# Performance work log

Hardware: AMD Instinct MI355X
Metric: run time of the kernel (lower is better)

Reference implementation:

```python
import jax, jax.numpy as jnp
import numpy as np

N_NODES = 20000
N_EDGES = 160000
D_IN = 512
D_OUT = 64


def _propagate(x, src, dst, num_nodes):
    # SLPropagate with add_self_loops=False, normalize=False:
    # out[dst] += x[src]  (plain sum aggregation over incoming edges)
    return jax.ops.segment_sum(x[src], dst, num_segments=num_nodes)


def setup_inputs() -> dict:
    key = jax.random.key(0)
    k1, k2, k3, k4 = jax.random.split(key, 4)
    x = jax.random.normal(k1, (N_NODES, D_IN), dtype=jnp.float32)
    edge_index = jax.random.randint(k2, (2, N_EDGES), 0, N_NODES, dtype=jnp.int64)
    # torch.nn.Linear default init scale ~ 1/sqrt(fan_in)
    s = 1.0 / np.sqrt(D_IN)
    W1 = jax.random.uniform(k3, (D_IN, D_IN), dtype=jnp.float32, minval=-s, maxval=s)
    W2 = jax.random.uniform(k4, (D_OUT, D_IN), dtype=jnp.float32, minval=-s, maxval=s)
    return {"x": x, "edge_index": edge_index, "W1": W1, "W2": W2}


def reference(x, edge_index, W1, W2):
    num_nodes = x.shape[0]
    src, dst = edge_index[0], edge_index[1]
    h = _propagate(x, src, dst, num_nodes)          # [N, D_IN]
    h = jax.nn.relu(jnp.einsum('nd,ed->ne', h, W1))  # lin1 (no bias) + relu
    h = _propagate(h, src, dst, num_nodes)          # [N, D_IN]
    h = jnp.einsum('nd,od->no', h, W2)              # lin2 (no bias) -> [N, D_OUT]
    return jax.nn.log_softmax(h, axis=1)
```

## Files before the change

kernel.cpp:

```cpp
#include <hip/hip_runtime.h>

#define D 512
#define DOUT 64

typedef __bf16 bf16x8 __attribute__((ext_vector_type(8)));
typedef float floatx4 __attribute__((ext_vector_type(4)));

__device__ __forceinline__ void async_cp16(const void* g, void* lds) {
    __builtin_amdgcn_global_load_lds(
        (__attribute__((address_space(1))) void*)(void*)g,
        (__attribute__((address_space(3))) void*)lds, 16, 0, 0);
}

__global__ __launch_bounds__(256) void misc_kernel(
        const int* __restrict__ dst, int* __restrict__ deg, int nE, int degBlocks,
        const float* __restrict__ x, __bf16* __restrict__ xb, int xN8,
        const float* __restrict__ W1, __bf16* __restrict__ w1b, int w1N8,
        const float* __restrict__ W2, __bf16* __restrict__ w2b, int w2N8) {
    int b = blockIdx.x;
    if (b < degBlocks) {
        int e = b * 256 + threadIdx.x;
        if (e < nE) atomicAdd(&deg[dst[e]], 1);
        return;
    }
    b -= degBlocks;
    int xBlocks = (xN8 + 255) >> 8;
    int w1Blocks = (w1N8 + 255) >> 8;
    const float* in; __bf16* outp; int n8;
    if (b < xBlocks) { in = x; outp = xb; n8 = xN8; }
    else if (b < xBlocks + w1Blocks) { b -= xBlocks; in = W1; outp = w1b; n8 = w1N8; }
    else { b -= xBlocks + w1Blocks; in = W2; outp = w2b; n8 = w2N8; }
    int i = b * 256 + threadIdx.x;
    if (i < n8) {
        const float4* p = (const float4*)in + (size_t)i * 2;
        float4 v0 = p[0], v1 = p[1];
        bf16x8 o;
        o[0] = (__bf16)v0.x; o[1] = (__bf16)v0.y; o[2] = (__bf16)v0.z; o[3] = (__bf16)v0.w;
        o[4] = (__bf16)v1.x; o[5] = (__bf16)v1.y; o[6] = (__bf16)v1.z; o[7] = (__bf16)v1.w;
        *((bf16x8*)outp + i) = o;
    }
}

__global__ __launch_bounds__(1024) void exscan_kernel(const int* __restrict__ deg,
                                                      int* __restrict__ rp,
                                                      int* __restrict__ cursor, int n) {
    __shared__ int wtot[16];
    __shared__ int carry;
    int tid = threadIdx.x, lane = tid & 63, wid = tid >> 6;
    if (tid == 0) carry = 0;
    __syncthreads();
    for (int base = 0; base < n; base += 4096) {
        int i4 = base + tid * 4;
        int4 v = make_int4(0, 0, 0, 0);
        if (i4 + 3 < n) v = *(const int4*)(deg + i4);
        else {
            if (i4 + 0 < n) v.x = deg[i4 + 0];
            if (i4 + 1 < n) v.y = deg[i4 + 1];
            if (i4 + 2 < n) v.z = deg[i4 + 2];
            if (i4 + 3 < n) v.w = deg[i4 + 3];
        }
        int tsum = v.x + v.y + v.z + v.w;
        int s = tsum;
        #pragma unroll
        for (int off = 1; off < 64; off <<= 1) {
            int t = __shfl_up(s, off, 64);
            if (lane >= off) s += t;
        }
        if (lane == 63) wtot[wid] = s;
        __syncthreads();
        if (wid == 0 && lane < 16) {
            int wv = wtot[lane];
            int ws_ = wv;
            #pragma unroll
            for (int off = 1; off < 16; off <<= 1) {
                int t = __shfl_up(ws_, off, 64);
                if (lane >= off) ws_ += t;
            }
            wtot[lane] = ws_ - wv;
        }
        __syncthreads();
        int excl = carry + wtot[wid] + (s - tsum);
        int4 o;
        o.x = excl; o.y = o.x + v.x; o.z = o.y + v.y; o.w = o.z + v.z;
        if (i4 + 3 < n) {
            *(int4*)(rp + i4) = o;
            *(int4*)(cursor + i4) = o;
        } else {
            if (i4 + 0 < n) { rp[i4 + 0] = o.x; cursor[i4 + 0] = o.x; }
            if (i4 + 1 < n) { rp[i4 + 1] = o.y; cursor[i4 + 1] = o.y; }
            if (i4 + 2 < n) { rp[i4 + 2] = o.z; cursor[i4 + 2] = o.z; }
            if (i4 + 3 < n) { rp[i4 + 3] = o.w; cursor[i4 + 3] = o.w; }
        }
        __syncthreads();
        if (tid == 1023) carry = o.w + v.w;
        __syncthreads();
    }
    if (tid == 0) rp[n] = carry;
}

__global__ void fill_kernel(const int* __restrict__ src, const int* __restrict__ dst,
                            int* __restrict__ cursor, int* __restrict__ col, int nE) {
    int e = blockIdx.x * blockDim.x + threadIdx.x;
    if (e < nE) {
        int d = dst[e];
        int p = atomicAdd(&cursor[d], 1);
        col[p] = src[e];
    }
}

template<int BM, int BN, int WR, int WC, bool RELU>
__global__ __launch_bounds__(256) void gemm_mfma_nt(
        const __bf16* __restrict__ A, const __bf16* __restrict__ B,
        __bf16* __restrict__ Cout, int M, int N, int K) {
    constexpr int BK = 32;
    constexpr int WM = BM / WR, WN = BN / WC;
    constexpr int MI = WM / 16, NI = WN / 16;
    constexpr int CPA = BM / 64, CPB = BN / 64;

    __shared__ __bf16 As[4 * BM * 8];
    __shared__ __bf16 Bs[4 * BN * 8];

    const int tid = threadIdx.x;
    const int w = tid >> 6, lane = tid & 63;
    const int wrow = w / WC, wcol = w % WC;
    const int m0 = blockIdx.y * BM, n0 = blockIdx.x * BN;
    const int quad = lane >> 4, l15 = lane & 15;

    floatx4 acc[MI][NI] = {};

    for (int k0 = 0; k0 < K; k0 += BK) {
        #pragma unroll
        for (int c = 0; c < CPA; ++c) {
            int ca = w * CPA + c;
            int kq = ca / CPA;
            int row = m0 + (ca % CPA) * 64 + lane;
            if (row > M - 1) row = M - 1;
            async_cp16(A + (size_t)row * K + k0 + kq * 8, &As[(size_t)ca * 512]);
        }
        #pragma unroll
        for (int c = 0; c < CPB; ++c) {
            int cb = w * CPB + c;
            int kq = cb / CPB;
            int nn = n0 + (cb % CPB) * 64 + lane;
            async_cp16(B + (size_t)nn * K + k0 + kq * 8, &Bs[(size_t)cb * 512]);
        }
        __syncthreads();

        bf16x8 af[MI], bfr[NI];
        #pragma unroll
        for (int mi = 0; mi < MI; ++mi)
            af[mi] = *(const bf16x8*)&As[(size_t)(quad * BM + wrow * WM + mi * 16 + l15) * 8];
        #pragma unroll
        for (int nj = 0; nj < NI; ++nj)
            bfr[nj] = *(const bf16x8*)&Bs[(size_t)(quad * BN + wcol * WN + nj * 16 + l15) * 8];
        #pragma unroll
        for (int mi = 0; mi < MI; ++mi)
            #pragma unroll
            for (int nj = 0; nj < NI; ++nj)
                acc[mi][nj] = __builtin_amdgcn_mfma_f32_16x16x32_bf16(
                    af[mi], bfr[nj], acc[mi][nj], 0, 0, 0);
        __syncthreads();
    }

    #pragma unroll
    for (int mi = 0; mi < MI; ++mi) {
        #pragma unroll
        for (int r = 0; r < 4; ++r) {
            int m = m0 + wrow * WM + mi * 16 + quad * 4 + r;
            if (m < M) {
                #pragma unroll
                for (int nj = 0; nj < NI; ++nj) {
                    int n = n0 + wcol * WN + nj * 16 + l15;
                    float v = acc[mi][nj][r];
                    if (RELU) v = fmaxf(v, 0.f);
                    Cout[(size_t)m * N + n] = (__bf16)v;
                }
            }
        }
    }
}

__global__ __launch_bounds__(256) void prop1_gemm2(
        const __bf16* __restrict__ t, const int* __restrict__ rp,
        const int* __restrict__ col, const __bf16* __restrict__ B,
        __bf16* __restrict__ u, int nN) {
    __shared__ __bf16 As[32 * 512];
    __shared__ __bf16 Bs[4 * 64 * 8];

    const int tid = threadIdx.x;
    const int w = tid >> 6, lane = tid & 63;
    const int quad = lane >> 4, l15 = lane & 15;
    const int wrow = w >> 1, wcol = w & 1;
    const int m0 = blockIdx.x * 32;

    for (int r = w; r < 32; r += 4) {
        int n = m0 + r;
        float acc0[8] = {}, acc1[8] = {};
        if (n < nN) {
            int s0 = rp[n], s1 = rp[n + 1];
            int e = s0;
            for (; e + 4 <= s1; e += 4) {
                int sa = col[e], sb = col[e + 1], sc = col[e + 2], sd = col[e + 3];
                bf16x8 va = *(const bf16x8*)(t + (size_t)sa * D + lane * 8);
                bf16x8 vb = *(const bf16x8*)(t + (size_t)sb * D + lane * 8);
                bf16x8 vc = *(const bf16x8*)(t + (size_t)sc * D + lane * 8);
                bf16x8 vd = *(const bf16x8*)(t + (size_t)sd * D + lane * 8);
                #pragma unroll
                for (int i = 0; i < 8; ++i) {
                    acc0[i] += (float)va[i] + (float)vc[i];
                    acc1[i] += (float)vb[i] + (float)vd[i];
                }
            }
            for (; e < s1; ++e) {
                int sa = col[e];
                bf16x8 va = *(const bf16x8*)(t + (size_t)sa * D + lane * 8);
                #pragma unroll
                for (int i = 0; i < 8; ++i) acc0[i] += (float)va[i];
            }
        }
        bf16x8 o;
        #pragma unroll
        for (int i = 0; i < 8; ++i) o[i] = (__bf16)fmaxf(acc0[i] + acc1[i], 0.f);
        int P = r * 64 + ((lane + r) & 63);
        *(bf16x8*)&As[(size_t)P * 8] = o;
    }
    __syncthreads();

    floatx4 acc[2] = {};
    for (int k0 = 0; k0 < D; k0 += 32) {
        async_cp16(B + (size_t)lane * D + k0 + w * 8, &Bs[(size_t)w * 512]);
        __syncthreads();
        int g = (k0 >> 3) + quad;
        int row = wrow * 16 + l15;
        bf16x8 af = *(const bf16x8*)&As[(size_t)(row * 64 + ((g + row) & 63)) * 8];
        #pragma unroll
        for (int nj = 0; nj < 2; ++nj) {
            bf16x8 bfr = *(const bf16x8*)&Bs[(size_t)(quad * 64 + wcol * 32 + nj * 16 + l15) * 8];
            acc[nj] = __builtin_amdgcn_mfma_f32_16x16x32_bf16(af, bfr, acc[nj], 0, 0, 0);
        }
        __syncthreads();
    }

    #pragma unroll
    for (int r = 0; r < 4; ++r) {
        int m = m0 + wrow * 16 + quad * 4 + r;
        if (m < nN) {
            #pragma unroll
            for (int nj = 0; nj < 2; ++nj)
                u[(size_t)m * DOUT + wcol * 32 + nj * 16 + l15] = (__bf16)acc[nj][r];
        }
    }
}

__global__ __launch_bounds__(256) void prop2_lsm(const __bf16* __restrict__ u,
        const int* __restrict__ rp, const int* __restrict__ col,
        float* __restrict__ out, int nN) {
    int n = blockIdx.x * 4 + (threadIdx.x >> 6);
    if (n >= nN) return;
    int lane = threadIdx.x & 63;
    int s0 = rp[n], s1 = rp[n + 1];
    float a0 = 0.f, a1 = 0.f, a2 = 0.f, a3 = 0.f;
    int e = s0;
    for (; e + 4 <= s1; e += 4) {
        int sa = col[e], sb = col[e + 1], sc = col[e + 2], sd = col[e + 3];
        a0 += (float)u[(size_t)sa * DOUT + lane];
        a1 += (float)u[(size_t)sb * DOUT + lane];
        a2 += (float)u[(size_t)sc * DOUT + lane];
        a3 += (float)u[(size_t)sd * DOUT + lane];
    }
    for (; e < s1; ++e) a0 += (float)u[(size_t)col[e] * DOUT + lane];
    float v = (a0 + a2) + (a1 + a3);
    float mx = v;
    #pragma unroll
    for (int off = 32; off >= 1; off >>= 1) mx = fmaxf(mx, __shfl_xor(mx, off, 64));
    float s = expf(v - mx);
    #pragma unroll
    for (int off = 32; off >= 1; off >>= 1) s += __shfl_xor(s, off, 64);
    out[(size_t)n * DOUT + lane] = v - mx - logf(s);
}


extern "C" void kernel_launch(void* const* d_in, const int* in_sizes, int n_in,
                              void* d_out, int out_size, void* d_ws, size_t ws_size,
                              hipStream_t stream) {
    const float* x  = (const float*)d_in[0];
    const int*   ei = (const int*)d_in[1];
    const float* W1 = (const float*)d_in[2];
    const float* W2 = (const float*)d_in[3];
    float* out = (float*)d_out;

    const int N = in_sizes[0] / D;
    const int E = in_sizes[1] / 2;
    const int* src = ei;
    const int* dst = ei + E;

    size_t off = 0;
    auto alloc = [&](size_t bytes) -> void* {
        void* p = (char*)d_ws + off;
        off = (off + bytes + 255) & ~(size_t)255;
        return p;
    };
    int*    deg     = (int*)alloc(sizeof(int) * (size_t)N);
    int*    row_ptr = (int*)alloc(sizeof(int) * (size_t)(N + 1));
    int*    cursor  = (int*)alloc(sizeof(int) * (size_t)N);
    int*    col     = (int*)alloc(sizeof(int) * (size_t)E);
    __bf16* w1b     = (__bf16*)alloc(sizeof(__bf16) * (size_t)D * D);
    __bf16* w2b     = (__bf16*)alloc(sizeof(__bf16) * (size_t)DOUT * D);
    __bf16* xb      = (__bf16*)alloc(sizeof(__bf16) * (size_t)N * D);
    __bf16* t       = (__bf16*)alloc(sizeof(__bf16) * (size_t)N * D);
    __bf16* u       = (__bf16*)alloc(sizeof(__bf16) * (size_t)N * DOUT);

    const int degBlocks = (E + 255) / 256;
    const int xN8 = N * D / 8, w1N8 = D * D / 8, w2N8 = DOUT * D / 8;
    const int cvtBlocks = (xN8 + 255) / 256 + (w1N8 + 255) / 256 + (w2N8 + 255) / 256;

    hipMemsetAsync(deg, 0, sizeof(int) * (size_t)N, stream);
    misc_kernel<<<degBlocks + cvtBlocks, 256, 0, stream>>>(
        dst, deg, E, degBlocks, x, xb, xN8, W1, w1b, w1N8, W2, w2b, w2N8);
    exscan_kernel<<<1, 1024, 0, stream>>>(deg, row_ptr, cursor, N);
    fill_kernel<<<(E + 255) / 256, 256, 0, stream>>>(src, dst, cursor, col, E);

    dim3 g1(D / 128, (N + 127) / 128);
    gemm_mfma_nt<128, 128, 2, 2, false><<<g1, 256, 0, stream>>>(xb, w1b, t, N, D, D);
    prop1_gemm2<<<(N + 31) / 32, 256, 0, stream>>>(t, row_ptr, col, w2b, u, N);
    prop2_lsm<<<(N + 3) / 4, 256, 0, stream>>>(u, row_ptr, col, out, N);
}
```

Measured before the change: 186.0 us.

## Fold degree histogram into GEMM1 launch and halve prop1 tile rows

Replaces the memset with in-kernel zeroing of the degree array inside the conversion kernel. The edge-degree histogram moves out of the conversion kernel into extra blocks of the first GEMM launch, so the atomics overlap with MFMA work. The GEMM is also flattened to a 1D grid. The fused propagate+GEMM2 kernel now handles 16 nodes per block instead of 32, giving twice as many blocks and less LDS per block, at the cost of reloading W2 tiles more often.

```diff
diff --git a/kernel.cpp b/kernel.cpp
--- a/kernel.cpp
+++ b/kernel.cpp
@@ -12,18 +12,23 @@
         (__attribute__((address_space(3))) void*)lds, 16, 0, 0);
 }
 
-__global__ __launch_bounds__(256) void misc_kernel(
-        const int* __restrict__ dst, int* __restrict__ deg, int nE, int degBlocks,
+__global__ __launch_bounds__(256) void prep_kernel(
+        int* __restrict__ deg, int nN, int zeroBlocks,
         const float* __restrict__ x, __bf16* __restrict__ xb, int xN8,
         const float* __restrict__ W1, __bf16* __restrict__ w1b, int w1N8,
         const float* __restrict__ W2, __bf16* __restrict__ w2b, int w2N8) {
     int b = blockIdx.x;
-    if (b < degBlocks) {
-        int e = b * 256 + threadIdx.x;
-        if (e < nE) atomicAdd(&deg[dst[e]], 1);
+    if (b < zeroBlocks) {
+        int i4 = b * 1024 + threadIdx.x * 4;
+        if (i4 + 3 < nN) *(int4*)(deg + i4) = make_int4(0, 0, 0, 0);
+        else {
+            if (i4 + 0 < nN) deg[i4 + 0] = 0;
+            if (i4 + 1 < nN) deg[i4 + 1] = 0;
+            if (i4 + 2 < nN) deg[i4 + 2] = 0;
+        }
         return;
     }
-    b -= degBlocks;
+    b -= zeroBlocks;
     int xBlocks = (xN8 + 255) >> 8;
     int w1Blocks = (w1N8 + 255) >> 8;
     const float* in; __bf16* outp; int n8;
@@ -108,51 +113,57 @@
     }
 }
 
-template<int BM, int BN, int WR, int WC, bool RELU>
-__global__ __launch_bounds__(256) void gemm_mfma_nt(
+__global__ __launch_bounds__(256) void gemm1_hist(
         const __bf16* __restrict__ A, const __bf16* __restrict__ B,
-        __bf16* __restrict__ Cout, int M, int N, int K) {
-    constexpr int BK = 32;
-    constexpr int WM = BM / WR, WN = BN / WC;
-    constexpr int MI = WM / 16, NI = WN / 16;
-    constexpr int CPA = BM / 64, CPB = BN / 64;
+        __bf16* __restrict__ Cout, int M, int gemmBlocks,
+        const int* __restrict__ dst, int* __restrict__ deg, int nE) {
+    constexpr int BM = 128, BN = 128, BK = 32;
+    constexpr int MI = 4, NI = 4;
+    constexpr int CPA = 2, CPB = 2;
+
+    if (blockIdx.x >= gemmBlocks) {
+        int base = (blockIdx.x - gemmBlocks) * 256 + threadIdx.x;
+        int stride = (gridDim.x - gemmBlocks) * 256;
+        for (int e = base; e < nE; e += stride) atomicAdd(&deg[dst[e]], 1);
+        return;
+    }
 
     __shared__ __bf16 As[4 * BM * 8];
     __shared__ __bf16 Bs[4 * BN * 8];
 
     const int tid = threadIdx.x;
     const int w = tid >> 6, lane = tid & 63;
-    const int wrow = w / WC, wcol = w % WC;
-    const int m0 = blockIdx.y * BM, n0 = blockIdx.x * BN;
+    const int wrow = w >> 1, wcol = w & 1;
+    const int m0 = (blockIdx.x >> 2) * BM, n0 = (blockIdx.x & 3) * BN;
     const int quad = lane >> 4, l15 = lane & 15;
 
     floatx4 acc[MI][NI] = {};
 
-    for (int k0 = 0; k0 < K; k0 += BK) {
+    for (int k0 = 0; k0 < D; k0 += BK) {
         #pragma unroll
         for (int c = 0; c < CPA; ++c) {
             int ca = w * CPA + c;
             int kq = ca / CPA;
             int row = m0 + (ca % CPA) * 64 + lane;
             if (row > M - 1) row = M - 1;
-            async_cp16(A + (size_t)row * K + k0 + kq * 8, &As[(size_t)ca * 512]);
+            async_cp16(A + (size_t)row * D + k0 + kq * 8, &As[(size_t)ca * 512]);
         }
         #pragma unroll
         for (int c = 0; c < CPB; ++c) {
             int cb = w * CPB + c;
             int kq = cb / CPB;
             int nn = n0 + (cb % CPB) * 64 + lane;
-            async_cp16(B + (size_t)nn * K + k0 + kq * 8, &Bs[(size_t)cb * 512]);
+            async_cp16(B + (size_t)nn * D + k0 + kq * 8, &Bs[(size_t)cb * 512]);
         }
         __syncthreads();
 
         bf16x8 af[MI], bfr[NI];
         #pragma unroll
         for (int mi = 0; mi < MI; ++mi)
-            af[mi] = *(const bf16x8*)&As[(size_t)(quad * BM + wrow * WM + mi * 16 + l15) * 8];
+            af[mi] = *(const bf16x8*)&As[(size_t)(quad * BM + wrow * 64 + mi * 16 + l15) * 8];
         #pragma unroll
         for (int nj = 0; nj < NI; ++nj)
-            bfr[nj] = *(const bf16x8*)&Bs[(size_t)(quad * BN + wcol * WN + nj * 16 + l15) * 8];
+            bfr[nj] = *(const bf16x8*)&Bs[(size_t)(quad * BN + wcol * 64 + nj * 16 + l15) * 8];
         #pragma unroll
         for (int mi = 0; mi < MI; ++mi)
             #pragma unroll
@@ -166,14 +177,12 @@
     for (int mi = 0; mi < MI; ++mi) {
         #pragma unroll
         for (int r = 0; r < 4; ++r) {
-            int m = m0 + wrow * WM + mi * 16 + quad * 4 + r;
+            int m = m0 + wrow * 64 + mi * 16 + quad * 4 + r;
             if (m < M) {
                 #pragma unroll
                 for (int nj = 0; nj < NI; ++nj) {
-                    int n = n0 + wcol * WN + nj * 16 + l15;
-                    float v = acc[mi][nj][r];
-                    if (RELU) v = fmaxf(v, 0.f);
-                    Cout[(size_t)m * N + n] = (__bf16)v;
+                    int n = n0 + wcol * 64 + nj * 16 + l15;
+                    Cout[(size_t)m * D + n] = (__bf16)acc[mi][nj][r];
                 }
             }
         }
@@ -184,16 +193,15 @@
         const __bf16* __restrict__ t, const int* __restrict__ rp,
         const int* __restrict__ col, const __bf16* __restrict__ B,
         __bf16* __restrict__ u, int nN) {
-    __shared__ __bf16 As[32 * 512];
+    __shared__ __bf16 As[16 * 512];
     __shared__ __bf16 Bs[4 * 64 * 8];
 
     const int tid = threadIdx.x;
     const int w = tid >> 6, lane = tid & 63;
     const int quad = lane >> 4, l15 = lane & 15;
-    const int wrow = w >> 1, wcol = w & 1;
-    const int m0 = blockIdx.x * 32;
-
-    for (int r = w; r < 32; r += 4) {
+    const int m0 = blockIdx.x * 16;
+
+    for (int r = w; r < 16; r += 4) {
         int n = m0 + r;
         float acc0[8] = {}, acc1[8] = {};
         if (n < nN) {
@@ -226,29 +234,22 @@
     }
     __syncthreads();
 
-    floatx4 acc[2] = {};
+    floatx4 acc = {};
     for (int k0 = 0; k0 < D; k0 += 32) {
         async_cp16(B + (size_t)lane * D + k0 + w * 8, &Bs[(size_t)w * 512]);
         __syncthreads();
         int g = (k0 >> 3) + quad;
-        int row = wrow * 16 + l15;
-        bf16x8 af = *(const bf16x8*)&As[(size_t)(row * 64 + ((g + row) & 63)) * 8];
-        #pragma unroll
-        for (int nj = 0; nj < 2; ++nj) {
-            bf16x8 bfr = *(const bf16x8*)&Bs[(size_t)(quad * 64 + wcol * 32 + nj * 16 + l15) * 8];
-            acc[nj] = __builtin_amdgcn_mfma_f32_16x16x32_bf16(af, bfr, acc[nj], 0, 0, 0);
-        }
+        bf16x8 af = *(const bf16x8*)&As[(size_t)(l15 * 64 + ((g + l15) & 63)) * 8];
+        bf16x8 bfr = *(const bf16x8*)&Bs[(size_t)(quad * 64 + w * 16 + l15) * 8];
+        acc = __builtin_amdgcn_mfma_f32_16x16x32_bf16(af, bfr, acc, 0, 0, 0);
         __syncthreads();
     }
 
     #pragma unroll
     for (int r = 0; r < 4; ++r) {
-        int m = m0 + wrow * 16 + quad * 4 + r;
-        if (m < nN) {
-            #pragma unroll
-            for (int nj = 0; nj < 2; ++nj)
-                u[(size_t)m * DOUT + wcol * 32 + nj * 16 + l15] = (__bf16)acc[nj][r];
-        }
+        int m = m0 + quad * 4 + r;
+        if (m < nN)
+            u[(size_t)m * DOUT + w * 16 + l15] = (__bf16)acc[r];
     }
 }
 
@@ -310,18 +311,20 @@
     __bf16* t       = (__bf16*)alloc(sizeof(__bf16) * (size_t)N * D);
     __bf16* u       = (__bf16*)alloc(sizeof(__bf16) * (size_t)N * DOUT);
 
-    const int degBlocks = (E + 255) / 256;
+    const int zeroBlocks = (N + 1023) / 1024;
     const int xN8 = N * D / 8, w1N8 = D * D / 8, w2N8 = DOUT * D / 8;
     const int cvtBlocks = (xN8 + 255) / 256 + (w1N8 + 255) / 256 + (w2N8 + 255) / 256;
 
-    hipMemsetAsync(deg, 0, sizeof(int) * (size_t)N, stream);
-    misc_kernel<<<degBlocks + cvtBlocks, 256, 0, stream>>>(
-        dst, deg, E, degBlocks, x, xb, xN8, W1, w1b, w1N8, W2, w2b, w2N8);
+    prep_kernel<<<zeroBlocks + cvtBlocks, 256, 0, stream>>>(
+        deg, N, zeroBlocks, x, xb, xN8, W1, w1b, w1N8, W2, w2b, w2N8);
+
+    const int gemmBlocks = ((N + 127) / 128) * 4;
+    gemm1_hist<<<gemmBlocks + 64, 256, 0, stream>>>(
+        xb, w1b, t, N, gemmBlocks, dst, deg, E);
+
     exscan_kernel<<<1, 1024, 0, stream>>>(deg, row_ptr, cursor, N);
     fill_kernel<<<(E + 255) / 256, 256, 0, stream>>>(src, dst, cursor, col, E);
 
-    dim3 g1(D / 128, (N + 127) / 128);
-    gemm_mfma_nt<128, 128, 2, 2, false><<<g1, 256, 0, stream>>>(xb, w1b, t, N, D, D);
-    prop1_gemm2<<<(N + 31) / 32, 256, 0, stream>>>(t, row_ptr, col, w2b, u, N);
+    prop1_gemm2<<<(N + 15) / 16, 256, 0, stream>>>(t, row_ptr, col, w2b, u, N);
     prop2_lsm<<<(N + 3) / 4, 256, 0, stream>>>(u, row_ptr, col, out, N);
 }
```

Result: faster. 175.7 us (-5.5%).
